# Kernel tuning notes

Measured on AMD Instinct MI355X. Metric: run time of the kernel, lower is better.

Reference implementation:

```python
import jax, jax.numpy as jnp
import numpy as np

D_MODEL = 1024
N_HEADS = 16
D_HEAD = D_MODEL // N_HEADS
D_FF = 4096
EPS = 1e-5


def _layernorm(x, g, b):
    mu = jnp.mean(x, axis=-1, keepdims=True)
    var = jnp.mean(jnp.square(x - mu), axis=-1, keepdims=True)
    return (x - mu) * jax.lax.rsqrt(var + EPS) * g + b


def setup_inputs() -> dict:
    key = jax.random.key(0)
    ks = jax.random.split(key, 16)
    B, S, D = 2, 2048, D_MODEL

    def xavier(k, shape):
        fan_in, fan_out = shape[0], shape[1]
        lim = float(np.sqrt(6.0 / (fan_in + fan_out)))
        return jax.random.uniform(k, shape, jnp.float32, -lim, lim)

    return {
        "x": jax.random.normal(ks[0], (B, S, D), jnp.float32),
        "ln1_g": jnp.ones((D,), jnp.float32),
        "ln1_b": jnp.zeros((D,), jnp.float32),
        "wq": xavier(ks[1], (D, D)), "bq": jnp.zeros((D,), jnp.float32),
        "wk": xavier(ks[2], (D, D)), "bk": jnp.zeros((D,), jnp.float32),
        "wv": xavier(ks[3], (D, D)), "bv": jnp.zeros((D,), jnp.float32),
        "wo": xavier(ks[4], (D, D)), "bo": jnp.zeros((D,), jnp.float32),
        "wf": xavier(ks[5], (D, N_HEADS)), "bf": jnp.zeros((N_HEADS,), jnp.float32),
        "ln2_g": jnp.ones((D,), jnp.float32),
        "ln2_b": jnp.zeros((D,), jnp.float32),
        "w1": xavier(ks[6], (D, D_FF)), "b1": jnp.zeros((D_FF,), jnp.float32),
        "w2": xavier(ks[7], (D_FF, D)), "b2": jnp.zeros((D,), jnp.float32),
    }


def reference(x, ln1_g, ln1_b, wq, bq, wk, bk, wv, bv, wo, bo, wf, bf,
              ln2_g, ln2_b, w1, b1, w2, b2):
    B, S, D = x.shape
    H, Dh = N_HEADS, D_HEAD

    # --- pre-norm forgetting attention ---
    h = _layernorm(x, ln1_g, ln1_b)
    q = (h @ wq + bq).reshape(B, S, H, Dh)
    k = (h @ wk + bk).reshape(B, S, H, Dh)
    v = (h @ wv + bv).reshape(B, S, H, Dh)

    # per-head scalar forget gate f_t in (0,1); cumulative log-decay c_t
    logf = jax.nn.log_sigmoid(h @ wf + bf)           # (B, S, H)
    c = jnp.cumsum(logf, axis=1)                     # (B, S, H)

    scale = 1.0 / jnp.sqrt(jnp.asarray(Dh, x.dtype))
    logits = jnp.einsum("bihd,bjhd->bhij", q, k) * scale
    # decay bias D_ij = c_i - c_j (sum of log forget gates in (j, i])
    decay = c.transpose(0, 2, 1)                     # (B, H, S)
    logits = logits + decay[:, :, :, None] - decay[:, :, None, :]

    causal = jnp.tril(jnp.ones((S, S), bool))
    logits = jnp.where(causal[None, None], logits, -jnp.inf)

    attn = jax.nn.softmax(logits, axis=-1)           # (B, H, S, S)
    ctx = jnp.einsum("bhij,bjhd->bihd", attn, v).reshape(B, S, D)
    attn_out = ctx @ wo + bo

    x = x + attn_out                                 # dropout = identity (eval)

    # --- pre-norm GELU MLP ---
    h2 = _layernorm(x, ln2_g, ln2_b)
    ff = jax.nn.gelu(h2 @ w1 + b1, approximate=False) @ w2 + b2
    return x + ff
```

## Files before the change

kernel.cpp:

```cpp
#include <hip/hip_runtime.h>
#include <hip/hip_bf16.h>
#include <math.h>

typedef unsigned short u16;
typedef unsigned int u32;
typedef __bf16 bf16x8 __attribute__((ext_vector_type(8)));
typedef float f32x4 __attribute__((ext_vector_type(4)));
typedef u32 u32x4 __attribute__((ext_vector_type(4)));

__device__ __forceinline__ u16 f2bf(float f) {
  __hip_bfloat16 h = __float2bfloat16(f);
  return *reinterpret_cast<u16*>(&h);
}
__device__ __forceinline__ float bf2f(u16 u) {
  return __uint_as_float(((u32)u) << 16);
}

#define GLL(gp, lp)                                                     \
  __builtin_amdgcn_global_load_lds(                                     \
      (const __attribute__((address_space(1))) void*)(gp),              \
      (__attribute__((address_space(3))) void*)(lp), 16, 0, 0)

__global__ __launch_bounds__(256) void transpose_cast(
    const float* __restrict__ in, u16* __restrict__ out, int R, int C) {
  __shared__ float tile[32][33];
  int c0 = blockIdx.x * 32, r0 = blockIdx.y * 32;
  int tx = threadIdx.x & 31, ty = threadIdx.x >> 5;
  for (int i = ty; i < 32; i += 8) {
    int r = r0 + i, c = c0 + tx;
    if (r < R && c < C) tile[i][tx] = in[(size_t)r * C + c];
  }
  __syncthreads();
  for (int i = ty; i < 32; i += 8) {
    int c = c0 + i, r = r0 + tx;
    if (c < C && r < R) out[(size_t)c * R + r] = f2bf(tile[tx][i]);
  }
}

__global__ __launch_bounds__(256) void transpose_cast3(
    const float* __restrict__ in0, const float* __restrict__ in1,
    const float* __restrict__ in2, u16* __restrict__ out) {
  __shared__ float tile[32][33];
  const float* in = (blockIdx.z == 0) ? in0 : (blockIdx.z == 1) ? in1 : in2;
  u16* o = out + (size_t)blockIdx.z * 1024 * 1024;
  int c0 = blockIdx.x * 32, r0 = blockIdx.y * 32;
  int tx = threadIdx.x & 31, ty = threadIdx.x >> 5;
  for (int i = ty; i < 32; i += 8)
    tile[i][tx] = in[(size_t)(r0 + i) * 1024 + c0 + tx];
  __syncthreads();
  for (int i = ty; i < 32; i += 8)
    o[(size_t)(c0 + i) * 1024 + r0 + tx] = f2bf(tile[tx][i]);
}

__global__ __launch_bounds__(256) void pack3(
    const float* __restrict__ a, const float* __restrict__ b,
    const float* __restrict__ c, float* __restrict__ o, u32* __restrict__ ctr) {
  int t = blockIdx.x * 256 + threadIdx.x;
  if (t == 0) *ctr = 0u;
  if (t < 1024) o[t] = a[t];
  else if (t < 2048) o[t] = b[t - 1024];
  else if (t < 3072) o[t] = c[t - 2048];
}

__global__ __launch_bounds__(256) void ln_kernel(
    const float* x, const float* __restrict__ g,
    const float* __restrict__ bb, u16* __restrict__ out,
    float* xadd, const float* addb) {
  __shared__ float red[8];
  const int row = blockIdx.x;
  const float* xr = x + (size_t)row * 1024;
  f32x4 v = *(const f32x4*)(xr + threadIdx.x * 4);
  float s = v[0] + v[1] + v[2] + v[3];
  #pragma unroll
  for (int off = 32; off > 0; off >>= 1) s += __shfl_xor(s, off, 64);
  if ((threadIdx.x & 63) == 0) red[threadIdx.x >> 6] = s;
  __syncthreads();
  float mu = (red[0] + red[1] + red[2] + red[3]) * (1.0f / 1024.0f);
  f32x4 d;
  d[0] = v[0] - mu; d[1] = v[1] - mu; d[2] = v[2] - mu; d[3] = v[3] - mu;
  float sq = d[0]*d[0] + d[1]*d[1] + d[2]*d[2] + d[3]*d[3];
  #pragma unroll
  for (int off = 32; off > 0; off >>= 1) sq += __shfl_xor(sq, off, 64);
  if ((threadIdx.x & 63) == 0) red[4 + (threadIdx.x >> 6)] = sq;
  __syncthreads();
  float var = (red[4] + red[5] + red[6] + red[7]) * (1.0f / 1024.0f);
  float rstd = rsqrtf(var + 1e-5f);
  int cb = threadIdx.x * 4;
  #pragma unroll
  for (int e = 0; e < 4; ++e)
    out[(size_t)row * 1024 + cb + e] = f2bf(d[e] * rstd * g[cb + e] + bb[cb + e]);
  if (xadd) {
    f32x4 w;
    #pragma unroll
    for (int e = 0; e < 4; ++e) w[e] = v[e] + addb[cb + e];
    *(f32x4*)(xadd + (size_t)row * 1024 + cb) = w;
  }
}

__global__ __launch_bounds__(256) void gemm_bt(
    const u16* __restrict__ A, const u16* __restrict__ Bt,
    const float* __restrict__ bias, const float* __restrict__ res,
    void* __restrict__ outp, int M, int N, int K, int mode) {
  __shared__ u16 As[2 * 128 * 32];
  __shared__ u16 Bs[2 * 128 * 32];
  const int tid = threadIdx.x;
  const int m0 = blockIdx.y * 128, n0 = blockIdx.x * 128;
  const int wave = tid >> 6, lane = tid & 63;
  const int wm = (wave >> 1) * 64, wn = (wave & 1) * 64;
  const int lr = lane & 15, quad = lane >> 4;
  const int g0 = wave * 2;
  const int srow0 = g0 * 16 + (lane >> 2);
  const int scol = (lane & 3) * 8;
  const u16* Ag0 = A + (size_t)(m0 + srow0) * K + scol;
  const u16* Ag1 = A + (size_t)(m0 + srow0 + 16) * K + scol;
  const u16* Bg0 = Bt + (size_t)(n0 + srow0) * K + scol;
  const u16* Bg1 = Bt + (size_t)(n0 + srow0 + 16) * K + scol;
  const int ao0 = g0 * 512, ao1 = (g0 + 1) * 512;

  f32x4 acc[4][4] = {};

  GLL(Ag0, As + ao0);
  GLL(Ag1, As + ao1);
  GLL(Bg0, Bs + ao0);
  GLL(Bg1, Bs + ao1);
  __syncthreads();

  int cur = 0;
  for (int k0 = 0; k0 < K; k0 += 32) {
    const int cb = cur * 4096, nb = (cur ^ 1) * 4096;
    if (k0 + 32 < K) {
      GLL(Ag0 + k0 + 32, As + nb + ao0);
      GLL(Ag1 + k0 + 32, As + nb + ao1);
      GLL(Bg0 + k0 + 32, Bs + nb + ao0);
      GLL(Bg1 + k0 + 32, Bs + nb + ao1);
    }
    bf16x8 af[4], bfr[4];
    #pragma unroll
    for (int t = 0; t < 4; ++t) {
      af[t]  = *(const bf16x8*)&As[cb + (wm + t * 16 + lr) * 32 + quad * 8];
      bfr[t] = *(const bf16x8*)&Bs[cb + (wn + t * 16 + lr) * 32 + quad * 8];
    }
    #pragma unroll
    for (int mt = 0; mt < 4; ++mt)
      #pragma unroll
      for (int nt = 0; nt < 4; ++nt)
        acc[mt][nt] = __builtin_amdgcn_mfma_f32_16x16x32_bf16(
            af[mt], bfr[nt], acc[mt][nt], 0, 0, 0);
    __syncthreads();
    cur ^= 1;
  }

  #pragma unroll
  for (int mt = 0; mt < 4; ++mt) {
    #pragma unroll
    for (int nt = 0; nt < 4; ++nt) {
      const int col = n0 + wn + nt * 16 + lr;
      const float bvv = bias[col];
      #pragma unroll
      for (int rr = 0; rr < 4; ++rr) {
        const int row = m0 + wm + mt * 16 + quad * 4 + rr;
        const size_t idx = (size_t)row * N + col;
        float v = acc[mt][nt][rr] + bvv;
        if (mode == 0) {
          ((float*)outp)[idx] = v;
        } else if (mode == 1) {
          ((float*)outp)[idx] = v + res[idx];
        } else if (mode == 2) {
          float gl = 0.5f * v * (1.0f + erff(v * 0.70710678118654752f));
          ((u16*)outp)[idx] = f2bf(gl);
        } else {
          ((u16*)outp)[idx] = f2bf(v);
        }
      }
    }
  }
}

__global__ __launch_bounds__(256) void gemm_bt_sk(
    const u16* __restrict__ A, const u16* __restrict__ Bt,
    float* __restrict__ outp, int M, int N, int Ktot, int Kslice) {
  __shared__ u16 As[2 * 128 * 32];
  __shared__ u16 Bs[2 * 128 * 32];
  const int tid = threadIdx.x;
  const int m0 = blockIdx.y * 128, n0 = blockIdx.x * 128;
  const int kbeg = blockIdx.z * Kslice, kend = kbeg + Kslice;
  const int wave = tid >> 6, lane = tid & 63;
  const int wm = (wave >> 1) * 64, wn = (wave & 1) * 64;
  const int lr = lane & 15, quad = lane >> 4;
  const int g0 = wave * 2;
  const int srow0 = g0 * 16 + (lane >> 2);
  const int scol = (lane & 3) * 8;
  const u16* Ag0 = A + (size_t)(m0 + srow0) * Ktot + scol;
  const u16* Ag1 = A + (size_t)(m0 + srow0 + 16) * Ktot + scol;
  const u16* Bg0 = Bt + (size_t)(n0 + srow0) * Ktot + scol;
  const u16* Bg1 = Bt + (size_t)(n0 + srow0 + 16) * Ktot + scol;
  const int ao0 = g0 * 512, ao1 = (g0 + 1) * 512;

  f32x4 acc[4][4] = {};

  GLL(Ag0 + kbeg, As + ao0);
  GLL(Ag1 + kbeg, As + ao1);
  GLL(Bg0 + kbeg, Bs + ao0);
  GLL(Bg1 + kbeg, Bs + ao1);
  __syncthreads();

  int cur = 0;
  for (int k0 = kbeg; k0 < kend; k0 += 32) {
    const int cb = cur * 4096, nb = (cur ^ 1) * 4096;
    if (k0 + 32 < kend) {
      GLL(Ag0 + k0 + 32, As + nb + ao0);
      GLL(Ag1 + k0 + 32, As + nb + ao1);
      GLL(Bg0 + k0 + 32, Bs + nb + ao0);
      GLL(Bg1 + k0 + 32, Bs + nb + ao1);
    }
    bf16x8 af[4], bfr[4];
    #pragma unroll
    for (int t = 0; t < 4; ++t) {
      af[t]  = *(const bf16x8*)&As[cb + (wm + t * 16 + lr) * 32 + quad * 8];
      bfr[t] = *(const bf16x8*)&Bs[cb + (wn + t * 16 + lr) * 32 + quad * 8];
    }
    #pragma unroll
    for (int mt = 0; mt < 4; ++mt)
      #pragma unroll
      for (int nt = 0; nt < 4; ++nt)
        acc[mt][nt] = __builtin_amdgcn_mfma_f32_16x16x32_bf16(
            af[mt], bfr[nt], acc[mt][nt], 0, 0, 0);
    __syncthreads();
    cur ^= 1;
  }

  #pragma unroll
  for (int mt = 0; mt < 4; ++mt) {
    #pragma unroll
    for (int nt = 0; nt < 4; ++nt) {
      const int col = n0 + wn + nt * 16 + lr;
      #pragma unroll
      for (int rr = 0; rr < 4; ++rr) {
        const int row = m0 + wm + mt * 16 + quad * 4 + rr;
        __hip_atomic_fetch_add(&outp[(size_t)row * N + col], acc[mt][nt][rr],
                               __ATOMIC_RELAXED, __HIP_MEMORY_SCOPE_AGENT);
      }
    }
  }
}

__global__ __launch_bounds__(256) void gemm_n64(
    const u16* __restrict__ A, const u16* __restrict__ Bt,
    const float* __restrict__ bias, const float* __restrict__ res,
    void* __restrict__ outp, int M, int N, int K, int mode) {
  __shared__ u16 As[2 * 128 * 32];
  __shared__ u16 Bs[2 * 64 * 32];
  const int tid = threadIdx.x;
  const int m0 = blockIdx.y * 128, n0 = blockIdx.x * 64;
  const int wave = tid >> 6, lane = tid & 63;
  const int wm = (wave >> 1) * 64, wn = (wave & 1) * 32;
  const int lr = lane & 15, quad = lane >> 4;
  const int g0 = wave * 2;
  const int srow = lane >> 2;
  const int scol = (lane & 3) * 8;
  const u16* Ag0 = A + (size_t)(m0 + g0 * 16 + srow) * K + scol;
  const u16* Ag1 = A + (size_t)(m0 + g0 * 16 + 16 + srow) * K + scol;
  const u16* Bg  = Bt + (size_t)(n0 + wave * 16 + srow) * K + scol;
  const int ao0 = g0 * 512, ao1 = (g0 + 1) * 512, bo = wave * 512;

  f32x4 acc[4][2] = {};

  GLL(Ag0, As + ao0);
  GLL(Ag1, As + ao1);
  GLL(Bg, Bs + bo);
  __syncthreads();

  int cur = 0;
  for (int k0 = 0; k0 < K; k0 += 32) {
    const int cba = cur * 4096, nba = (cur ^ 1) * 4096;
    const int cbb = cur * 2048, nbb = (cur ^ 1) * 2048;
    if (k0 + 32 < K) {
      GLL(Ag0 + k0 + 32, As + nba + ao0);
      GLL(Ag1 + k0 + 32, As + nba + ao1);
      GLL(Bg + k0 + 32, Bs + nbb + bo);
    }
    bf16x8 af[4], bfr[2];
    #pragma unroll
    for (int t = 0; t < 4; ++t)
      af[t] = *(const bf16x8*)&As[cba + (wm + t * 16 + lr) * 32 + quad * 8];
    #pragma unroll
    for (int t = 0; t < 2; ++t)
      bfr[t] = *(const bf16x8*)&Bs[cbb + (wn + t * 16 + lr) * 32 + quad * 8];
    #pragma unroll
    for (int mt = 0; mt < 4; ++mt)
      #pragma unroll
      for (int nt = 0; nt < 2; ++nt)
        acc[mt][nt] = __builtin_amdgcn_mfma_f32_16x16x32_bf16(
            af[mt], bfr[nt], acc[mt][nt], 0, 0, 0);
    __syncthreads();
    cur ^= 1;
  }

  #pragma unroll
  for (int mt = 0; mt < 4; ++mt) {
    #pragma unroll
    for (int nt = 0; nt < 2; ++nt) {
      const int col = n0 + wn + nt * 16 + lr;
      const float bvv = bias[col];
      #pragma unroll
      for (int rr = 0; rr < 4; ++rr) {
        const int row = m0 + wm + mt * 16 + quad * 4 + rr;
        const size_t idx = (size_t)row * N + col;
        float v = acc[mt][nt][rr] + bvv;
        if (mode == 0) {
          ((float*)outp)[idx] = v;
        } else if (mode == 1) {
          ((float*)outp)[idx] = v + res[idx];
        } else if (mode == 2) {
          float gl = 0.5f * v * (1.0f + erff(v * 0.70710678118654752f));
          ((u16*)outp)[idx] = f2bf(gl);
        } else {
          ((u16*)outp)[idx] = f2bf(v);
        }
      }
    }
  }
}

__global__ __launch_bounds__(64) void logf_kernel(
    const u16* __restrict__ h, const u16* __restrict__ wfT,
    const float* __restrict__ bfv, float* __restrict__ c) {
  const int row = blockIdx.x;
  const int lane = threadIdx.x;
  float acc[16];
  #pragma unroll
  for (int n = 0; n < 16; ++n) acc[n] = 0.f;
  for (int t = 0; t < 16; ++t) {
    int kidx = t * 64 + lane;
    float hv = bf2f(h[(size_t)row * 1024 + kidx]);
    #pragma unroll
    for (int n = 0; n < 16; ++n)
      acc[n] += hv * bf2f(wfT[n * 1024 + kidx]);
  }
  float z = 0.f;
  #pragma unroll
  for (int n = 0; n < 16; ++n) {
    float r = acc[n];
    #pragma unroll
    for (int off = 1; off < 64; off <<= 1) r += __shfl_xor(r, off, 64);
    if (lane == n) z = r;
  }
  if (lane < 16) {
    z += bfv[lane];
    float lf = (z >= 0.f) ? -log1pf(expf(-z)) : (z - log1pf(expf(z)));
    c[(size_t)row * 16 + lane] = lf;
  }
}

__global__ __launch_bounds__(64) void cumsum_kernel(float* __restrict__ c, int S) {
  const int b = blockIdx.x >> 4, h = blockIdx.x & 15;
  const int lane = threadIdx.x;
  float carry = 0.f;
  for (int s0 = 0; s0 < S; s0 += 64) {
    float v = c[(size_t)(b * S + s0 + lane) * 16 + h];
    #pragma unroll
    for (int off = 1; off < 64; off <<= 1) {
      float t = __shfl_up(v, off, 64);
      if (lane >= off) v += t;
    }
    v += carry;
    c[(size_t)(b * S + s0 + lane) * 16 + h] = v;
    carry = __shfl(v, 63, 64);
  }
}

__global__ __launch_bounds__(256) void vtrans(
    const u16* __restrict__ qkvb, u16* __restrict__ vtg) {
  __shared__ u16 t[32][33];
  const int bh = blockIdx.z, b = bh >> 4, h = bh & 15;
  const int s0 = blockIdx.x * 32, d0 = blockIdx.y * 32;
  const int tx = threadIdx.x & 31, ty = threadIdx.x >> 5;
  for (int i = ty; i < 32; i += 8)
    t[i][tx] = qkvb[(size_t)(b * 2048 + s0 + i) * 3072 + 2048 + h * 64 + d0 + tx];
  __syncthreads();
  for (int i = ty; i < 32; i += 8)
    vtg[(size_t)(bh * 64 + d0 + i) * 2048 + s0 + tx] = t[tx][i];
}

__global__ __launch_bounds__(64) void qk_norms(
    const u16* __restrict__ qkvb, float* __restrict__ qkmax) {
  const int tile = blockIdx.x, bh = blockIdx.y, z = blockIdx.z;
  const int b = bh >> 4, h = bh & 15;
  const int tok = tile * 64 + (int)threadIdx.x;
  const u16* p = qkvb + (size_t)(b * 2048 + tok) * 3072 + z * 1024 + h * 64;
  float s = 0.f;
  #pragma unroll
  for (int i = 0; i < 4; ++i) {
    u32x4 w = *(const u32x4*)(p + i * 16);
    u32x4 w2 = *(const u32x4*)(p + i * 16 + 8);
    #pragma unroll
    for (int e = 0; e < 4; ++e) {
      float lo = __uint_as_float(w[e] << 16);
      float hi = __uint_as_float(w[e] & 0xffff0000u);
      float lo2 = __uint_as_float(w2[e] << 16);
      float hi2 = __uint_as_float(w2[e] & 0xffff0000u);
      s += lo * lo + hi * hi + lo2 * lo2 + hi2 * hi2;
    }
  }
  s = sqrtf(s);
  #pragma unroll
  for (int off = 1; off < 64; off <<= 1) s = fmaxf(s, __shfl_xor(s, off, 64));
  if (threadIdx.x == 0) qkmax[z * 1024 + bh * 32 + tile] = s;
}

#define FS 72
#define NITEMS 1024
#define L2E 1.4426950408889634f

__global__ __launch_bounds__(256) void fattn(
    const u16* __restrict__ qkvb, const u16* __restrict__ vtg,
    const float* __restrict__ c, const float* __restrict__ qkmax,
    u16* __restrict__ ctx, u32* __restrict__ ctr) {
  __shared__ u16 Qs[64 * FS];
  __shared__ u16 Ks[64 * FS];
  __shared__ u16 Vt[64 * FS];
  __shared__ u16 Ps[64 * FS];
  __shared__ float cjs[64];
  __shared__ float wmn[4];
  __shared__ u32 sh_item;
  const int S = 2048;
  const int tid = threadIdx.x, wave = tid >> 6, lane = tid & 63;
  const int lr = lane & 15, quad = lane >> 4;
  const int w16 = wave * 16;
  const int sr = tid >> 2, scc = (tid & 3) * 16;

  for (;;) {
    if (tid == 0) sh_item = atomicAdd(ctr, 1u);
    __syncthreads();
    const u32 item = sh_item;
    if (item >= NITEMS) return;
    const int qt = 31 - (int)(item >> 5);
    const int bh = (int)(item & 31), b = bh >> 4, h = bh & 15;
    const int i0 = qt * 64;

    {
      const u16* src = qkvb + (size_t)(b * S + i0 + sr) * 3072 + h * 64 + scc;
      *(u32x4*)&Qs[sr * FS + scc] = *(const u32x4*)src;
      *(u32x4*)&Qs[sr * FS + scc + 8] = *(const u32x4*)(src + 8);
    }
    u32x4 kr0, kr1, vr0, vr1;
    float cjr = 0.f;
    {
      const u16* ks = qkvb + (size_t)(b * S + i0 + sr) * 3072 + 1024 + h * 64 + scc;
      kr0 = *(const u32x4*)ks;
      kr1 = *(const u32x4*)(ks + 8);
      const u16* vs = vtg + (size_t)(bh * 64 + sr) * 2048 + i0 + scc;
      vr0 = *(const u32x4*)vs;
      vr1 = *(const u32x4*)(vs + 8);
      if (tid < 64) cjr = c[(size_t)(b * S + i0 + tid) * 16 + h];
    }
    float bscale;
    {
      float qm = qkmax[bh * 32 + qt];
      float km = 0.f;
      for (int t = 0; t <= qt; ++t) km = fmaxf(km, qkmax[1024 + bh * 32 + t]);
      bscale = qm * km * (0.125f * L2E);
    }
    float m_[4], l_[4], alpha[4];
    f32x4 o_[4];
    #pragma unroll
    for (int r = 0; r < 4; ++r) {
      m_[r] = -INFINITY;
      l_[r] = 0.f;
    }
    #pragma unroll
    for (int dt = 0; dt < 4; ++dt) o_[dt] = (f32x4){0.f, 0.f, 0.f, 0.f};

    __syncthreads();
    const bf16x8 aq0 = *(const bf16x8*)&Qs[(w16 + lr) * FS + quad * 8];
    const bf16x8 aq1 = *(const bf16x8*)&Qs[(w16 + lr) * FS + 32 + quad * 8];

    for (int jt = qt; jt >= 0; --jt) {
      const int j0 = jt * 64;
      *(u32x4*)&Ks[sr * FS + scc] = kr0;
      *(u32x4*)&Ks[sr * FS + scc + 8] = kr1;
      *(u32x4*)&Vt[sr * FS + scc] = vr0;
      *(u32x4*)&Vt[sr * FS + scc + 8] = vr1;
      if (tid < 64) cjs[tid] = cjr * L2E;
      if (jt > 0) {
        const int j1 = j0 - 64;
        const u16* ks = qkvb + (size_t)(b * S + j1 + sr) * 3072 + 1024 + h * 64 + scc;
        kr0 = *(const u32x4*)ks;
        kr1 = *(const u32x4*)(ks + 8);
        const u16* vs = vtg + (size_t)(bh * 64 + sr) * 2048 + j1 + scc;
        vr0 = *(const u32x4*)vs;
        vr1 = *(const u32x4*)(vs + 8);
        if (tid < 64) cjr = c[(size_t)(b * S + j1 + tid) * 16 + h];
      }
      __syncthreads();

      f32x4 sc[4];
      #pragma unroll
      for (int nt = 0; nt < 4; ++nt) {
        bf16x8 bk0 = *(const bf16x8*)&Ks[(nt * 16 + lr) * FS + quad * 8];
        bf16x8 bk1 = *(const bf16x8*)&Ks[(nt * 16 + lr) * FS + 32 + quad * 8];
        f32x4 z = {0.f, 0.f, 0.f, 0.f};
        z = __builtin_amdgcn_mfma_f32_16x16x32_bf16(aq0, bk0, z, 0, 0, 0);
        z = __builtin_amdgcn_mfma_f32_16x16x32_bf16(aq1, bk1, z, 0, 0, 0);
        sc[nt] = z;
      }
      const bool diag = (jt == qt);
      #pragma unroll
      for (int r = 0; r < 4; ++r) {
        const int i = i0 + w16 + quad * 4 + r;
        float lg[4], mrow = -INFINITY;
        #pragma unroll
        for (int nt = 0; nt < 4; ++nt) {
          const int j = j0 + nt * 16 + lr;
          float v = sc[nt][r] * (0.125f * L2E) - cjs[nt * 16 + lr];
          if (diag && (j > i)) v = -INFINITY;
          lg[nt] = v;
          mrow = fmaxf(mrow, v);
        }
        #pragma unroll
        for (int off = 1; off < 16; off <<= 1)
          mrow = fmaxf(mrow, __shfl_xor(mrow, off, 64));
        const float mn = fmaxf(m_[r], mrow);
        alpha[r] = __builtin_exp2f(m_[r] - mn);
        m_[r] = mn;
        float rs = 0.f;
        #pragma unroll
        for (int nt = 0; nt < 4; ++nt) {
          const float p = __builtin_exp2f(lg[nt] - mn);
          Ps[(w16 + quad * 4 + r) * FS + nt * 16 + lr] = f2bf(p);
          rs += p;
        }
        l_[r] = l_[r] * alpha[r] + rs;
      }
      asm volatile("s_waitcnt lgkmcnt(0)" ::: "memory");
      #pragma unroll
      for (int dt = 0; dt < 4; ++dt)
        #pragma unroll
        for (int r = 0; r < 4; ++r) o_[dt][r] *= alpha[r];
      bf16x8 ap0 = *(const bf16x8*)&Ps[(w16 + lr) * FS + quad * 8];
      bf16x8 ap1 = *(const bf16x8*)&Ps[(w16 + lr) * FS + 32 + quad * 8];
      #pragma unroll
      for (int dt = 0; dt < 4; ++dt) {
        bf16x8 bv0 = *(const bf16x8*)&Vt[(dt * 16 + lr) * FS + quad * 8];
        bf16x8 bv1 = *(const bf16x8*)&Vt[(dt * 16 + lr) * FS + 32 + quad * 8];
        o_[dt] = __builtin_amdgcn_mfma_f32_16x16x32_bf16(ap0, bv0, o_[dt], 0, 0, 0);
        o_[dt] = __builtin_amdgcn_mfma_f32_16x16x32_bf16(ap1, bv1, o_[dt], 0, 0, 0);
      }
      {
        float wmin = fminf(fminf(m_[0], m_[1]), fminf(m_[2], m_[3]));
        wmin = fminf(wmin, __shfl_xor(wmin, 16, 64));
        wmin = fminf(wmin, __shfl_xor(wmin, 32, 64));
        if (lane == 0) wmn[wave] = wmin;
      }
      __syncthreads();
      if (jt > 0) {
        const float bmin = fminf(fminf(wmn[0], wmn[1]), fminf(wmn[2], wmn[3]));
        const float cend = c[(size_t)(b * S + j0 - 1) * 16 + h];
        if (bscale - cend * L2E < bmin - 40.f) break;
      }
    }
    #pragma unroll
    for (int r = 0; r < 4; ++r) {
      float lt = l_[r];
      #pragma unroll
      for (int off = 1; off < 16; off <<= 1) lt += __shfl_xor(lt, off, 64);
      const float inv = 1.0f / lt;
      const size_t base = (size_t)(b * S + i0 + w16 + quad * 4 + r) * 1024 + h * 64;
      #pragma unroll
      for (int dt = 0; dt < 4; ++dt)
        ctx[base + dt * 16 + lr] = f2bf(o_[dt][r] * inv);
    }
  }
}

extern "C" void kernel_launch(void* const* d_in, const int* in_sizes, int n_in,
                              void* d_out, int out_size, void* d_ws, size_t ws_size,
                              hipStream_t stream) {
  const float* x    = (const float*)d_in[0];
  const float* ln1g = (const float*)d_in[1];
  const float* ln1b = (const float*)d_in[2];
  const float* wq   = (const float*)d_in[3];
  const float* bq   = (const float*)d_in[4];
  const float* wk   = (const float*)d_in[5];
  const float* bk   = (const float*)d_in[6];
  const float* wv   = (const float*)d_in[7];
  const float* bv   = (const float*)d_in[8];
  const float* wo   = (const float*)d_in[9];
  const float* bo   = (const float*)d_in[10];
  const float* wf   = (const float*)d_in[11];
  const float* bfv  = (const float*)d_in[12];
  const float* ln2g = (const float*)d_in[13];
  const float* ln2b = (const float*)d_in[14];
  const float* w1   = (const float*)d_in[15];
  const float* b1   = (const float*)d_in[16];
  const float* w2   = (const float*)d_in[17];
  const float* b2   = (const float*)d_in[18];
  float* out = (float*)d_out;

  char* ws = (char*)d_ws;
  const size_t MB = 1024 * 1024;
  u16*   wqkvT = (u16*)(ws + 0 * MB);
  u16*   woT   = (u16*)(ws + 6 * MB);
  u16*   w1T   = (u16*)(ws + 8 * MB);
  u16*   w2T   = (u16*)(ws + 16 * MB);
  u16*   wfT   = (u16*)(ws + 24 * MB);
  float* bqkv  = (float*)(ws + 24 * MB + 65536);
  u32*   fctr  = (u32*)(ws + 24 * MB + 131072);
  u16*   hbuf  = (u16*)(ws + 25 * MB);
  u16*   ctx   = (u16*)(ws + 33 * MB);
  u16*   qkvb  = (u16*)(ws + 41 * MB);
  u16*   vtg   = (u16*)(ws + 65 * MB);
  float* cb    = (float*)(ws + 73 * MB);
  float* qkmax = (float*)(ws + 73 * MB + 262144);
  u16*   act1  = (u16*)(ws + 74 * MB);

  dim3 blk(256);
  transpose_cast3<<<dim3(32, 32, 3), blk, 0, stream>>>(wq, wk, wv, wqkvT);
  transpose_cast<<<dim3(32, 32), blk, 0, stream>>>(wo, woT, 1024, 1024);
  transpose_cast<<<dim3(128, 32), blk, 0, stream>>>(w1, w1T, 1024, 4096);
  transpose_cast<<<dim3(32, 128), blk, 0, stream>>>(w2, w2T, 4096, 1024);
  transpose_cast<<<dim3(1, 32), blk, 0, stream>>>(wf, wfT, 1024, 16);
  pack3<<<12, blk, 0, stream>>>(bq, bk, bv, bqkv, fctr);
  ln_kernel<<<4096, blk, 0, stream>>>(x, ln1g, ln1b, hbuf, nullptr, nullptr);
  gemm_bt<<<dim3(24, 32), blk, 0, stream>>>(hbuf, wqkvT, bqkv, nullptr, qkvb,
                                            4096, 3072, 1024, 3);
  logf_kernel<<<4096, dim3(64), 0, stream>>>(hbuf, wfT, bfv, cb);
  cumsum_kernel<<<32, dim3(64), 0, stream>>>(cb, 2048);
  vtrans<<<dim3(64, 2, 32), blk, 0, stream>>>(qkvb, vtg);
  qk_norms<<<dim3(32, 32, 2), dim3(64), 0, stream>>>(qkvb, qkmax);
  fattn<<<dim3(1024), blk, 0, stream>>>(qkvb, vtg, cb, qkmax, ctx, fctr);
  gemm_n64<<<dim3(16, 32), blk, 0, stream>>>(ctx, woT, bo, x, out,
                                             4096, 1024, 1024, 1);
  ln_kernel<<<4096, blk, 0, stream>>>(out, ln2g, ln2b, hbuf, out, b2);
  gemm_bt<<<dim3(32, 32), blk, 0, stream>>>(hbuf, w1T, b1, nullptr, act1,
                                            4096, 4096, 1024, 2);
  gemm_bt_sk<<<dim3(8, 32, 4), blk, 0, stream>>>(act1, w2T, out,
                                                 4096, 1024, 4096, 1024);
}
```

Measured before the change: 481.1 us.

## Deepen GEMM LDS pipeline to four stages with one barrier per k-step

The three bf16 GEMM kernels now use a four-slot LDS ring instead of double buffering, prefetching two k-tiles ahead. Explicit vmcnt waits plus a single s_barrier per iteration replace the trailing __syncthreads, so global-to-LDS loads overlap with MFMA work for longer. The FFN down-projection split-K is also cut from 4 to 2 slices, which halves the atomic adds into the output. The cost is double the LDS per block, which may lower occupancy, and fewer blocks for the split-K GEMM. Overwriting slot st+2 while slower waves may still read slot st-2 relies on the single barrier being enough.

```diff
diff --git a/kernel.cpp b/kernel.cpp
--- a/kernel.cpp
+++ b/kernel.cpp
@@ -101,8 +101,8 @@
     const u16* __restrict__ A, const u16* __restrict__ Bt,
     const float* __restrict__ bias, const float* __restrict__ res,
     void* __restrict__ outp, int M, int N, int K, int mode) {
-  __shared__ u16 As[2 * 128 * 32];
-  __shared__ u16 Bs[2 * 128 * 32];
+  __shared__ u16 As[4 * 128 * 32];
+  __shared__ u16 Bs[4 * 128 * 32];
   const int tid = threadIdx.x;
   const int m0 = blockIdx.y * 128, n0 = blockIdx.x * 128;
   const int wave = tid >> 6, lane = tid & 63;
@@ -119,21 +119,29 @@
 
   f32x4 acc[4][4] = {};
 
-  GLL(Ag0, As + ao0);
-  GLL(Ag1, As + ao1);
-  GLL(Bg0, Bs + ao0);
-  GLL(Bg1, Bs + ao1);
-  __syncthreads();
-
-  int cur = 0;
+  GLL(Ag0, As + ao0); GLL(Ag1, As + ao1);
+  GLL(Bg0, Bs + ao0); GLL(Bg1, Bs + ao1);
+  if (K > 32) {
+    GLL(Ag0 + 32, As + 4096 + ao0); GLL(Ag1 + 32, As + 4096 + ao1);
+    GLL(Bg0 + 32, Bs + 4096 + ao0); GLL(Bg1 + 32, Bs + 4096 + ao1);
+  }
+
   for (int k0 = 0; k0 < K; k0 += 32) {
-    const int cb = cur * 4096, nb = (cur ^ 1) * 4096;
-    if (k0 + 32 < K) {
-      GLL(Ag0 + k0 + 32, As + nb + ao0);
-      GLL(Ag1 + k0 + 32, As + nb + ao1);
-      GLL(Bg0 + k0 + 32, Bs + nb + ao0);
-      GLL(Bg1 + k0 + 32, Bs + nb + ao1);
-    }
+    const int cb = ((k0 >> 5) & 3) * 4096;
+    if (k0 + 64 < K) {
+      const int pb = (((k0 >> 5) + 2) & 3) * 4096;
+      GLL(Ag0 + k0 + 64, As + pb + ao0);
+      GLL(Ag1 + k0 + 64, As + pb + ao1);
+      GLL(Bg0 + k0 + 64, Bs + pb + ao0);
+      GLL(Bg1 + k0 + 64, Bs + pb + ao1);
+      asm volatile("s_waitcnt vmcnt(8)" ::: "memory");
+    } else if (k0 + 32 < K) {
+      asm volatile("s_waitcnt vmcnt(4)" ::: "memory");
+    } else {
+      asm volatile("s_waitcnt vmcnt(0)" ::: "memory");
+    }
+    __builtin_amdgcn_s_barrier();
+    __builtin_amdgcn_sched_barrier(0);
     bf16x8 af[4], bfr[4];
     #pragma unroll
     for (int t = 0; t < 4; ++t) {
@@ -146,8 +154,6 @@
       for (int nt = 0; nt < 4; ++nt)
         acc[mt][nt] = __builtin_amdgcn_mfma_f32_16x16x32_bf16(
             af[mt], bfr[nt], acc[mt][nt], 0, 0, 0);
-    __syncthreads();
-    cur ^= 1;
   }
 
   #pragma unroll
@@ -179,8 +185,8 @@
 __global__ __launch_bounds__(256) void gemm_bt_sk(
     const u16* __restrict__ A, const u16* __restrict__ Bt,
     float* __restrict__ outp, int M, int N, int Ktot, int Kslice) {
-  __shared__ u16 As[2 * 128 * 32];
-  __shared__ u16 Bs[2 * 128 * 32];
+  __shared__ u16 As[4 * 128 * 32];
+  __shared__ u16 Bs[4 * 128 * 32];
   const int tid = threadIdx.x;
   const int m0 = blockIdx.y * 128, n0 = blockIdx.x * 128;
   const int kbeg = blockIdx.z * Kslice, kend = kbeg + Kslice;
@@ -198,21 +204,30 @@
 
   f32x4 acc[4][4] = {};
 
-  GLL(Ag0 + kbeg, As + ao0);
-  GLL(Ag1 + kbeg, As + ao1);
-  GLL(Bg0 + kbeg, Bs + ao0);
-  GLL(Bg1 + kbeg, Bs + ao1);
-  __syncthreads();
-
-  int cur = 0;
+  GLL(Ag0 + kbeg, As + ao0); GLL(Ag1 + kbeg, As + ao1);
+  GLL(Bg0 + kbeg, Bs + ao0); GLL(Bg1 + kbeg, Bs + ao1);
+  if (kbeg + 32 < kend) {
+    GLL(Ag0 + kbeg + 32, As + 4096 + ao0); GLL(Ag1 + kbeg + 32, As + 4096 + ao1);
+    GLL(Bg0 + kbeg + 32, Bs + 4096 + ao0); GLL(Bg1 + kbeg + 32, Bs + 4096 + ao1);
+  }
+
   for (int k0 = kbeg; k0 < kend; k0 += 32) {
-    const int cb = cur * 4096, nb = (cur ^ 1) * 4096;
-    if (k0 + 32 < kend) {
-      GLL(Ag0 + k0 + 32, As + nb + ao0);
-      GLL(Ag1 + k0 + 32, As + nb + ao1);
-      GLL(Bg0 + k0 + 32, Bs + nb + ao0);
-      GLL(Bg1 + k0 + 32, Bs + nb + ao1);
-    }
+    const int st = (k0 - kbeg) >> 5;
+    const int cb = (st & 3) * 4096;
+    if (k0 + 64 < kend) {
+      const int pb = ((st + 2) & 3) * 4096;
+      GLL(Ag0 + k0 + 64, As + pb + ao0);
+      GLL(Ag1 + k0 + 64, As + pb + ao1);
+      GLL(Bg0 + k0 + 64, Bs + pb + ao0);
+      GLL(Bg1 + k0 + 64, Bs + pb + ao1);
+      asm volatile("s_waitcnt vmcnt(8)" ::: "memory");
+    } else if (k0 + 32 < kend) {
+      asm volatile("s_waitcnt vmcnt(4)" ::: "memory");
+    } else {
+      asm volatile("s_waitcnt vmcnt(0)" ::: "memory");
+    }
+    __builtin_amdgcn_s_barrier();
+    __builtin_amdgcn_sched_barrier(0);
     bf16x8 af[4], bfr[4];
     #pragma unroll
     for (int t = 0; t < 4; ++t) {
@@ -225,8 +240,6 @@
       for (int nt = 0; nt < 4; ++nt)
         acc[mt][nt] = __builtin_amdgcn_mfma_f32_16x16x32_bf16(
             af[mt], bfr[nt], acc[mt][nt], 0, 0, 0);
-    __syncthreads();
-    cur ^= 1;
   }
 
   #pragma unroll
@@ -248,8 +261,8 @@
     const u16* __restrict__ A, const u16* __restrict__ Bt,
     const float* __restrict__ bias, const float* __restrict__ res,
     void* __restrict__ outp, int M, int N, int K, int mode) {
-  __shared__ u16 As[2 * 128 * 32];
-  __shared__ u16 Bs[2 * 64 * 32];
+  __shared__ u16 As[4 * 128 * 32];
+  __shared__ u16 Bs[4 * 64 * 32];
   const int tid = threadIdx.x;
   const int m0 = blockIdx.y * 128, n0 = blockIdx.x * 64;
   const int wave = tid >> 6, lane = tid & 63;
@@ -265,20 +278,28 @@
 
   f32x4 acc[4][2] = {};
 
-  GLL(Ag0, As + ao0);
-  GLL(Ag1, As + ao1);
-  GLL(Bg, Bs + bo);
-  __syncthreads();
-
-  int cur = 0;
+  GLL(Ag0, As + ao0); GLL(Ag1, As + ao1); GLL(Bg, Bs + bo);
+  if (K > 32) {
+    GLL(Ag0 + 32, As + 4096 + ao0); GLL(Ag1 + 32, As + 4096 + ao1);
+    GLL(Bg + 32, Bs + 2048 + bo);
+  }
+
   for (int k0 = 0; k0 < K; k0 += 32) {
-    const int cba = cur * 4096, nba = (cur ^ 1) * 4096;
-    const int cbb = cur * 2048, nbb = (cur ^ 1) * 2048;
-    if (k0 + 32 < K) {
-      GLL(Ag0 + k0 + 32, As + nba + ao0);
-      GLL(Ag1 + k0 + 32, As + nba + ao1);
-      GLL(Bg + k0 + 32, Bs + nbb + bo);
-    }
+    const int st = k0 >> 5;
+    const int cba = (st & 3) * 4096, cbb = (st & 3) * 2048;
+    if (k0 + 64 < K) {
+      const int pba = ((st + 2) & 3) * 4096, pbb = ((st + 2) & 3) * 2048;
+      GLL(Ag0 + k0 + 64, As + pba + ao0);
+      GLL(Ag1 + k0 + 64, As + pba + ao1);
+      GLL(Bg + k0 + 64, Bs + pbb + bo);
+      asm volatile("s_waitcnt vmcnt(6)" ::: "memory");
+    } else if (k0 + 32 < K) {
+      asm volatile("s_waitcnt vmcnt(3)" ::: "memory");
+    } else {
+      asm volatile("s_waitcnt vmcnt(0)" ::: "memory");
+    }
+    __builtin_amdgcn_s_barrier();
+    __builtin_amdgcn_sched_barrier(0);
     bf16x8 af[4], bfr[2];
     #pragma unroll
     for (int t = 0; t < 4; ++t)
@@ -292,8 +313,6 @@
       for (int nt = 0; nt < 2; ++nt)
         acc[mt][nt] = __builtin_amdgcn_mfma_f32_16x16x32_bf16(
             af[mt], bfr[nt], acc[mt][nt], 0, 0, 0);
-    __syncthreads();
-    cur ^= 1;
   }
 
   #pragma unroll
@@ -634,6 +653,6 @@
   ln_kernel<<<4096, blk, 0, stream>>>(out, ln2g, ln2b, hbuf, out, b2);
   gemm_bt<<<dim3(32, 32), blk, 0, stream>>>(hbuf, w1T, b1, nullptr, act1,
                                             4096, 4096, 1024, 2);
-  gemm_bt_sk<<<dim3(8, 32, 4), blk, 0, stream>>>(act1, w2T, out,
-                                                 4096, 1024, 4096, 1024);
-}
+  gemm_bt_sk<<<dim3(8, 32, 2), blk, 0, stream>>>(act1, w2T, out,
+                                                 4096, 1024, 4096, 2048);
+}
```

Result: faster. 470.9 us (-2.1%).
